# Performance work log

Hardware: AMD Instinct MI355X
Metric: run time of the kernel (lower is better)

The kernel has to match this reference:

```python
import jax, jax.numpy as jnp
import numpy as np

# Hard-coded backbone constants from the original module
N_INIT = np.array([17.047, 14.099, 3.625], dtype=np.float32)
CA_INIT = np.array([16.967, 12.784, 4.338], dtype=np.float32)
C_INIT = np.array([15.685, 12.755, 5.133], dtype=np.float32)
LEN_C_N, LEN_N_CA, LEN_CA_C = 1.34, 1.46, 1.54
ANG_C_N = 115.0 / 180.0 * np.pi
ANG_N_CA = 121.0 / 180.0 * np.pi
ANG_CA_C = 109.0 / 180.0 * np.pi


def _unit(x):
    return x / jnp.linalg.norm(x, axis=-1, keepdims=True)


def _place_dihedral(a, b, c, bond_angle, bond_length, torsion):
    # a,b,c: [B,3]; torsion: [B]; bond_angle/bond_length: python floats
    ab = b - a
    bc = _unit(c - b)
    n = _unit(jnp.cross(ab, bc))
    nbc = jnp.cross(n, bc)
    d0 = -bond_length * jnp.cos(bond_angle)              # scalar
    d1 = bond_length * jnp.cos(torsion) * jnp.sin(bond_angle)  # [B]
    d2 = bond_length * jnp.sin(torsion) * jnp.sin(bond_angle)  # [B]
    # d = m^T @ [d0,d1,d2] with m rows = (bc, nbc, n)
    return c + d0 * bc + d1[:, None] * nbc + d2[:, None] * n


def setup_inputs() -> dict:
    key = jax.random.key(0)
    k1, k2, k3 = jax.random.split(key, 3)
    B, L = 4096, 512
    return {
        "phi": jax.random.normal(k1, (B, L), dtype=jnp.float32),
        "psi": jax.random.normal(k2, (B, L), dtype=jnp.float32),
        "omega": jax.random.normal(k3, (B, L), dtype=jnp.float32),
        "max_length": 512,
    }


def reference(phi, psi, omega, max_length):
    B, L = phi.shape
    steps = min(L - 1, max_length - 1)
    # initial N, CA, C coords repeated over batch: each [B,3]
    a0 = jnp.broadcast_to(jnp.asarray(N_INIT), (B, 3))
    b0 = jnp.broadcast_to(jnp.asarray(CA_INIT), (B, 3))
    c0 = jnp.broadcast_to(jnp.asarray(C_INIT), (B, 3))

    # per-step torsions: psi_i, omega_i, phi_{i+1}
    xs = (psi[:, :steps].T, omega[:, :steps].T, phi[:, 1:steps + 1].T)  # each [steps,B]

    def step(carry, tors):
        a, b, c = carry
        t_psi, t_omega, t_phi = tors
        d_n = _place_dihedral(a, b, c, ANG_C_N, LEN_C_N, t_psi)
        d_ca = _place_dihedral(b, c, d_n, ANG_N_CA, LEN_N_CA, t_omega)
        d_c = _place_dihedral(c, d_n, d_ca, ANG_CA_C, LEN_CA_C, t_phi)
        return (d_n, d_ca, d_c), jnp.stack([d_n, d_ca, d_c], axis=0)

    _, ys = jax.lax.scan(step, (a0, b0, c0), xs)  # ys: [steps,3,B,3]
    new_coords = jnp.transpose(ys, (2, 0, 1, 3)).reshape(B, 3 * steps, 3)
    init = jnp.stack([a0, b0, c0], axis=1)  # [B,3,3]
    return jnp.concatenate([init, new_coords], axis=1)  # [B, 3*(steps+1), 3]
```

## Files before the change

kernel.cpp:

```cpp
#include <hip/hip_runtime.h>


struct V3 { float x, y, z; };

__device__ __forceinline__ V3 vsub(V3 a, V3 b){ return {a.x-b.x, a.y-b.y, a.z-b.z}; }
__device__ __forceinline__ V3 vcross(V3 a, V3 b){
    return {a.y*b.z - a.z*b.y, a.z*b.x - a.x*b.z, a.x*b.y - a.y*b.x};
}
__device__ __forceinline__ float vdot(V3 a, V3 b){ return a.x*b.x + a.y*b.y + a.z*b.z; }
__device__ __forceinline__ V3 vunit(V3 a){
    float r = rsqrtf(vdot(a,a));
    return {a.x*r, a.y*r, a.z*r};
}

struct Xform { V3 c0, c1, c2, t; };

__device__ __forceinline__ V3 xrot(const Xform& X, V3 p){
    return { X.c0.x*p.x + X.c1.x*p.y + X.c2.x*p.z,
             X.c0.y*p.x + X.c1.y*p.y + X.c2.y*p.z,
             X.c0.z*p.x + X.c1.z*p.y + X.c2.z*p.z };
}
__device__ __forceinline__ V3 xapply(const Xform& X, V3 p){
    V3 r = xrot(X, p);
    return { r.x + X.t.x, r.y + X.t.y, r.z + X.t.z };
}
__device__ __forceinline__ Xform xcompose(const Xform& A, const Xform& B){
    Xform R;
    R.c0 = xrot(A, B.c0);
    R.c1 = xrot(A, B.c1);
    R.c2 = xrot(A, B.c2);
    R.t  = xapply(A, B.t);
    return R;
}

__device__ __forceinline__ Xform frame_of(V3 A, V3 B, V3 C){
    V3 bc  = vunit(vsub(C, B));
    V3 n   = vunit(vcross(vsub(B, A), bc));
    V3 nbc = vcross(n, bc);
    return { bc, nbc, n, C };
}

__device__ __forceinline__ Xform shfl_up_xf(const Xform& X, int d){
    Xform R;
    R.c0.x = __shfl_up(X.c0.x, d); R.c0.y = __shfl_up(X.c0.y, d); R.c0.z = __shfl_up(X.c0.z, d);
    R.c1.x = __shfl_up(X.c1.x, d); R.c1.y = __shfl_up(X.c1.y, d); R.c1.z = __shfl_up(X.c1.z, d);
    R.c2.x = __shfl_up(X.c2.x, d); R.c2.y = __shfl_up(X.c2.y, d); R.c2.z = __shfl_up(X.c2.z, d);
    R.t.x  = __shfl_up(X.t.x,  d); R.t.y  = __shfl_up(X.t.y,  d); R.t.z  = __shfl_up(X.t.z,  d);
    return R;
}

#define D0_CN   0.56630847f
#define LS_CN   1.21445243f
#define D0_NCA  0.75195559f
#define LS_NCA  1.25146426f
#define D0_CAC  0.50137496f
#define LS_CAC  1.45609861f

#define A0X (-2.0153295f)
#define A0Y ( 1.3804571f)

#define NIX 17.047f
#define NIY 14.099f
#define NIZ  3.625f
#define CAX 16.967f
#define CAY 12.784f
#define CAZ  4.338f
#define CIX 15.685f
#define CIY 12.755f
#define CIZ  5.133f

__device__ __forceinline__ V3 place_dihedral(V3 a, V3 b, V3 c,
                                             float d0, float Ls, float tor){
    V3 ab = vsub(b, a);
    V3 bc = vunit(vsub(c, b));
    V3 n  = vunit(vcross(ab, bc));
    V3 nbc = vcross(n, bc);
    float sn, cs;
    __sincosf(tor, &sn, &cs);
    float d1 = Ls * cs;
    float d2 = Ls * sn;
    return { c.x + d0*bc.x + d1*nbc.x + d2*n.x,
             c.y + d0*bc.y + d1*nbc.y + d2*n.y,
             c.z + d0*bc.z + d1*nbc.z + d2*n.z };
}

__device__ __forceinline__ void step3(V3& A, V3& B, V3& C,
                                      float tpsi, float tome, float tphi){
    V3 dn  = place_dihedral(A, B, C,  D0_CN,  LS_CN,  tpsi);
    V3 dca = place_dihedral(B, C, dn, D0_NCA, LS_NCA, tome);
    V3 dc  = place_dihedral(C, dn, dca, D0_CAC, LS_CAC, tphi);
    A = dn; B = dca; C = dc;
}

__device__ __forceinline__ int swz(int F){ return F ^ (((F >> 8) & 7) << 2); }

__device__ __forceinline__ void stage_row(float* lds, int r, V3 a, V3 b, V3 c){
    int base = r * 9;
    lds[swz(base+0)] = a.x; lds[swz(base+1)] = a.y; lds[swz(base+2)] = a.z;
    lds[swz(base+3)] = b.x; lds[swz(base+4)] = b.y; lds[swz(base+5)] = b.z;
    lds[swz(base+6)] = c.x; lds[swz(base+7)] = c.y; lds[swz(base+8)] = c.z;
}

__global__ __launch_bounds__(64, 2)
void nerf_wave(const float* __restrict__ phi,
               const float* __restrict__ psi,
               const float* __restrict__ omega,
               float* __restrict__ out,
               int steps){
    const int L = 512;
    const int S = 8;
    int b = blockIdx.x;
    int k = threadIdx.x;
    int s0 = k * S;

    __shared__ float lds[4608];

    const float* pphi = phi   + (size_t)b * L;
    const float* ppsi = psi   + (size_t)b * L;
    const float* pome = omega + (size_t)b * L;

    float4 ps0 = ((const float4*)(ppsi + s0))[0];
    float4 ps1 = ((const float4*)(ppsi + s0))[1];
    float4 om0 = ((const float4*)(pome + s0))[0];
    float4 om1 = ((const float4*)(pome + s0))[1];
    float4 ph0 = ((const float4*)(pphi + s0))[0];
    float4 ph1 = ((const float4*)(pphi + s0))[1];
    float phi8 = __shfl_down(ph0.x, 1);

    float tpsi[8] = {ps0.x, ps0.y, ps0.z, ps0.w, ps1.x, ps1.y, ps1.z, ps1.w};
    float tome[8] = {om0.x, om0.y, om0.z, om0.w, om1.x, om1.y, om1.z, om1.w};
    float tphi[8] = {ph0.y, ph0.z, ph0.w, ph1.x, ph1.y, ph1.z, ph1.w, phi8};

    V3 A, Bv, C;
    if (k == 0){
        A = {NIX, NIY, NIZ}; Bv = {CAX, CAY, CAZ}; C = {CIX, CIY, CIZ};
    } else {
        A = {A0X, A0Y, 0.f}; Bv = {-1.54f, 0.f, 0.f}; C = {0.f, 0.f, 0.f};
    }
    V3 locA[8], locB[8], locC[8];
    #pragma unroll
    for (int s = 0; s < 8; ++s){
        if (s0 + s < steps)
            step3(A, Bv, C, tpsi[s], tome[s], tphi[s]);
        locA[s] = A; locB[s] = Bv; locC[s] = C;
    }
    Xform V = frame_of(A, Bv, C);

    #pragma unroll
    for (int d = 1; d < 64; d <<= 1){
        Xform Pr = shfl_up_xf(V, d);
        if (k >= d) V = xcompose(Pr, V);
    }
    Xform Wp = shfl_up_xf(V, 1);

    if (k == 0){
        stage_row(lds, 0, {NIX, NIY, NIZ}, {CAX, CAY, CAZ}, {CIX, CIY, CIZ});
        #pragma unroll
        for (int s = 0; s < 8; ++s)
            stage_row(lds, s + 1, locA[s], locB[s], locC[s]);
    } else {
        #pragma unroll
        for (int s = 0; s < 8; ++s){
            if (s0 + s < steps)
                stage_row(lds, s0 + s + 1,
                          xapply(Wp, locA[s]), xapply(Wp, locB[s]), xapply(Wp, locC[s]));
        }
    }
    __syncthreads();

    float4* ol = (float4*)(out + (size_t)b * 4608u);
    const float4* ls = (const float4*)lds;
    #pragma unroll
    for (int i = 0; i < 18; ++i){
        int q = i * 64 + k;
        ol[q] = ls[q ^ ((q >> 6) & 7)];
    }
}

__global__ void nerf_seq_kernel(const float* __restrict__ phi,
                                const float* __restrict__ psi,
                                const float* __restrict__ omega,
                                float* __restrict__ out,
                                int B, int L, int steps){
    int b = blockIdx.x * blockDim.x + threadIdx.x;
    if (b >= B) return;
    V3 A  = {NIX, NIY, NIZ};
    V3 Bv = {CAX, CAY, CAZ};
    V3 C  = {CIX, CIY, CIZ};
    float* o = out + (size_t)b * 9u * (size_t)(steps + 1);
    o[0]=A.x;  o[1]=A.y;  o[2]=A.z;
    o[3]=Bv.x; o[4]=Bv.y; o[5]=Bv.z;
    o[6]=C.x;  o[7]=C.y;  o[8]=C.z;
    const float* pphi = phi   + (size_t)b * L;
    const float* ppsi = psi   + (size_t)b * L;
    const float* pome = omega + (size_t)b * L;
    for (int s = 0; s < steps; ++s){
        step3(A, Bv, C, ppsi[s], pome[s], pphi[s + 1]);
        float* os = o + 9u * (size_t)(s + 1);
        os[0]=A.x;  os[1]=A.y;  os[2]=A.z;
        os[3]=Bv.x; os[4]=Bv.y; os[5]=Bv.z;
        os[6]=C.x;  os[7]=C.y;  os[8]=C.z;
    }
}

extern "C" void kernel_launch(void* const* d_in, const int* in_sizes, int n_in,
                              void* d_out, int out_size, void* d_ws, size_t ws_size,
                              hipStream_t stream) {
    const float* phi   = (const float*)d_in[0];
    const float* psi   = (const float*)d_in[1];
    const float* omega = (const float*)d_in[2];
    float* out = (float*)d_out;

    const int L = 512;
    int B = in_sizes[0] / L;
    int steps = out_size / (9 * B) - 1;

    if (steps == 511 && in_sizes[0] == B * 512) {
        nerf_wave<<<B, 64, 0, stream>>>(phi, psi, omega, out, steps);
    } else {
        int block = 64;
        int grid = (B + block - 1) / block;
        nerf_seq_kernel<<<grid, block, 0, stream>>>(phi, psi, omega, out, B, L, steps);
    }
}
```

Before: 34.26 us.

## Stage output in two half-size LDS passes with float4 writes to raise occupancy

Halves the shared-memory staging buffer to 576 float4 and writes the output in two passes. Lanes 0-31 stage first, then lanes 32-63, with extra barriers between the passes. Each lane now packs its rows as aligned float4 stores, taking the previous lane's last coordinates through a shuffle instead of using scalar swizzled stores. Launch bounds go from 2 to 4 waves per unit. The aim is higher occupancy and fewer LDS store instructions, at the cost of extra syncs and serialised output phases.

```diff
diff --git a/kernel.cpp b/kernel.cpp
--- a/kernel.cpp
+++ b/kernel.cpp
@@ -92,28 +92,36 @@
     A = dn; B = dca; C = dc;
 }
 
-__device__ __forceinline__ int swz(int F){ return F ^ (((F >> 8) & 7) << 2); }
-
-__device__ __forceinline__ void stage_row(float* lds, int r, V3 a, V3 b, V3 c){
-    int base = r * 9;
-    lds[swz(base+0)] = a.x; lds[swz(base+1)] = a.y; lds[swz(base+2)] = a.z;
-    lds[swz(base+3)] = b.x; lds[swz(base+4)] = b.y; lds[swz(base+5)] = b.z;
-    lds[swz(base+6)] = c.x; lds[swz(base+7)] = c.y; lds[swz(base+8)] = c.z;
-}
-
-__global__ __launch_bounds__(64, 2)
-void nerf_wave(const float* __restrict__ phi,
+__device__ __forceinline__ void put4(float4* lds4, int p, float4 v){
+    lds4[p ^ ((p >> 6) & 7)] = v;
+}
+
+__device__ __forceinline__ void stage36(float4* lds4, int p,
+    V3 aA, V3 aB, V3 aC, V3 bA, V3 bB, V3 bC,
+    V3 cA, V3 cB, V3 cC, V3 dA, V3 dB, V3 dC){
+    put4(lds4, p+0, make_float4(aA.x, aA.y, aA.z, aB.x));
+    put4(lds4, p+1, make_float4(aB.y, aB.z, aC.x, aC.y));
+    put4(lds4, p+2, make_float4(aC.z, bA.x, bA.y, bA.z));
+    put4(lds4, p+3, make_float4(bB.x, bB.y, bB.z, bC.x));
+    put4(lds4, p+4, make_float4(bC.y, bC.z, cA.x, cA.y));
+    put4(lds4, p+5, make_float4(cA.z, cB.x, cB.y, cB.z));
+    put4(lds4, p+6, make_float4(cC.x, cC.y, cC.z, dA.x));
+    put4(lds4, p+7, make_float4(dA.y, dA.z, dB.x, dB.y));
+    put4(lds4, p+8, make_float4(dB.z, dC.x, dC.y, dC.z));
+}
+
+__global__ __launch_bounds__(64, 4)
+void nerf_half(const float* __restrict__ phi,
                const float* __restrict__ psi,
                const float* __restrict__ omega,
                float* __restrict__ out,
                int steps){
     const int L = 512;
-    const int S = 8;
     int b = blockIdx.x;
     int k = threadIdx.x;
-    int s0 = k * S;
-
-    __shared__ float lds[4608];
+    int s0 = k * 8;
+
+    __shared__ float4 lds4[576];
 
     const float* pphi = phi   + (size_t)b * L;
     const float* ppsi = psi   + (size_t)b * L;
@@ -153,27 +161,52 @@
     }
     Xform Wp = shfl_up_xf(V, 1);
 
-    if (k == 0){
-        stage_row(lds, 0, {NIX, NIY, NIZ}, {CAX, CAY, CAZ}, {CIX, CIY, CIZ});
-        #pragma unroll
-        for (int s = 0; s < 8; ++s)
-            stage_row(lds, s + 1, locA[s], locB[s], locC[s]);
-    } else {
+    if (k != 0){
         #pragma unroll
         for (int s = 0; s < 8; ++s){
-            if (s0 + s < steps)
-                stage_row(lds, s0 + s + 1,
-                          xapply(Wp, locA[s]), xapply(Wp, locB[s]), xapply(Wp, locC[s]));
+            locA[s] = xapply(Wp, locA[s]);
+            locB[s] = xapply(Wp, locB[s]);
+            locC[s] = xapply(Wp, locC[s]);
         }
     }
+
+    V3 nA, nB, nC;
+    nA.x = __shfl_up(locA[7].x, 1); nA.y = __shfl_up(locA[7].y, 1); nA.z = __shfl_up(locA[7].z, 1);
+    nB.x = __shfl_up(locB[7].x, 1); nB.y = __shfl_up(locB[7].y, 1); nB.z = __shfl_up(locB[7].z, 1);
+    nC.x = __shfl_up(locC[7].x, 1); nC.y = __shfl_up(locC[7].y, 1); nC.z = __shfl_up(locC[7].z, 1);
+    if (k == 0){
+        nA = {NIX, NIY, NIZ}; nB = {CAX, CAY, CAZ}; nC = {CIX, CIY, CIZ};
+    }
+
+    int m = k & 31;
+    int p0 = 18 * m;
+    float4* o4 = (float4*)(out + (size_t)b * 4608u);
+
+    if (k < 32){
+        stage36(lds4, p0,     nA, nB, nC, locA[0], locB[0], locC[0],
+                              locA[1], locB[1], locC[1], locA[2], locB[2], locC[2]);
+        stage36(lds4, p0 + 9, locA[3], locB[3], locC[3], locA[4], locB[4], locC[4],
+                              locA[5], locB[5], locC[5], locA[6], locB[6], locC[6]);
+    }
     __syncthreads();
-
-    float4* ol = (float4*)(out + (size_t)b * 4608u);
-    const float4* ls = (const float4*)lds;
-    #pragma unroll
-    for (int i = 0; i < 18; ++i){
+    #pragma unroll
+    for (int i = 0; i < 9; ++i){
         int q = i * 64 + k;
-        ol[q] = ls[q ^ ((q >> 6) & 7)];
+        o4[q] = lds4[q ^ ((q >> 6) & 7)];
+    }
+    __syncthreads();
+
+    if (k >= 32){
+        stage36(lds4, p0,     nA, nB, nC, locA[0], locB[0], locC[0],
+                              locA[1], locB[1], locC[1], locA[2], locB[2], locC[2]);
+        stage36(lds4, p0 + 9, locA[3], locB[3], locC[3], locA[4], locB[4], locC[4],
+                              locA[5], locB[5], locC[5], locA[6], locB[6], locC[6]);
+    }
+    __syncthreads();
+    #pragma unroll
+    for (int i = 0; i < 9; ++i){
+        int q = i * 64 + k;
+        o4[576 + q] = lds4[q ^ ((q >> 6) & 7)];
     }
 }
 
@@ -216,7 +249,7 @@
     int steps = out_size / (9 * B) - 1;
 
     if (steps == 511 && in_sizes[0] == B * 512) {
-        nerf_wave<<<B, 64, 0, stream>>>(phi, psi, omega, out, steps);
+        nerf_half<<<B, 64, 0, stream>>>(phi, psi, omega, out, steps);
     } else {
         int block = 64;
         int grid = (B + block - 1) / block;
```

Result: slower. 45.40 us (+32.5%).
